# Kernel tuning notes

Hardware: AMD Instinct MI355X
Metric: run time of the kernel (lower is better)

## Reference

```python
import jax, jax.numpy as jnp
import numpy as np

N, E, H, NH, HD = 16384, 131072, 128, 8, 16
CUTOFF = 5.0
PATCH = H // 2  # 64, aggregation_custom effective patch dim


def setup_inputs() -> dict:
    key = jax.random.key(0)
    ks = jax.random.split(key, 24)
    w = lambda k, s: (jax.random.normal(k, s, dtype=jnp.float32) * 0.05)
    d = jax.random.normal(ks[5], (E, 3), dtype=jnp.float32)
    d = d / (jnp.linalg.norm(d, axis=-1, keepdims=True) + 1e-8)  # unit directions
    return {
        "x": jax.random.normal(ks[0], (N, H), dtype=jnp.float32),
        "vec": jax.random.normal(ks[1], (N, 3, H), dtype=jnp.float32),
        "edge_index": jax.random.randint(ks[2], (2, E), 0, N),
        "r_ij": jax.random.uniform(ks[3], (E,), dtype=jnp.float32) * CUTOFF,
        "f_ij": jax.random.normal(ks[4], (E, H), dtype=jnp.float32),
        "d_ij": d,
        "ln_g": jnp.ones((H,), jnp.float32), "ln_b": jnp.zeros((H,), jnp.float32),
        "Wq": w(ks[6], (H, H)), "bq": jnp.zeros((H,), jnp.float32),
        "Wk": w(ks[7], (H, H)), "bk": jnp.zeros((H,), jnp.float32),
        "Wv": w(ks[8], (H, H)), "bv": jnp.zeros((H,), jnp.float32),
        "Wdk": w(ks[9], (H, H)), "bdk": jnp.zeros((H,), jnp.float32),
        "Wdv": w(ks[10], (H, H)), "bdv": jnp.zeros((H,), jnp.float32),
        "Wvec": w(ks[11], (3 * H, H)),
        "Ws": w(ks[12], (2 * H, H)), "bs": jnp.zeros((2 * H,), jnp.float32),
        "Wo": w(ks[13], (3 * H, H)), "bo": jnp.zeros((3 * H,), jnp.float32),
        "Wf": w(ks[14], (H, H)), "bf": jnp.zeros((H,), jnp.float32),
        "Wwsrc": w(ks[15], (H, H)), "Wwtrg": w(ks[16], (H, H)),
        "Wagg": w(ks[17], (H, PATCH)),  # fc_all: Linear(64 -> 128, no bias)
        "agg_param": jnp.full((1,), 1e-5, dtype=jnp.float32),
    }


def _cutoff(r):
    return 0.5 * (jnp.cos(jnp.pi * r / CUTOFF) + 1.0) * (r < CUTOFF).astype(r.dtype)


def _vector_rejection(v, d):
    # v: [E,3,H], d: [E,3]
    proj = (v * d[:, :, None]).sum(axis=1, keepdims=True)  # [E,1,H]
    return v - proj * d[:, :, None]


def reference(x, vec, edge_index, r_ij, f_ij, d_ij, ln_g, ln_b,
              Wq, bq, Wk, bk, Wv, bv, Wdk, bdk, Wdv, bdv, Wvec,
              Ws, bs, Wo, bo, Wf, bf, Wwsrc, Wwtrg, Wagg, agg_param):
    silu = jax.nn.silu
    n = x.shape[0]
    # LayerNorm on x; VecLayerNorm with norm_type='none', trainable=False is identity
    mu = x.mean(-1, keepdims=True)
    var = ((x - mu) ** 2).mean(-1, keepdims=True)
    xn = (x - mu) / jnp.sqrt(var + 1e-5) * ln_g + ln_b

    q = (xn @ Wq.T + bq).reshape(n, NH, HD)
    k = (xn @ Wk.T + bk).reshape(n, NH, HD)
    v = (xn @ Wv.T + bv).reshape(n, NH, HD)
    dk = silu(f_ij @ Wdk.T + bdk).reshape(-1, NH, HD)
    dv = silu(f_ij @ Wdv.T + bdv).reshape(-1, NH, HD)

    vec1, vec2, vec3 = jnp.split(jnp.einsum('nch,oh->nco', vec, Wvec), 3, axis=-1)
    vec_dot = (vec1 * vec2).sum(axis=1)  # [N,H]

    src, dst = edge_index[0], edge_index[1]  # j, i
    # --- message ---
    attn = (q[dst] * k[src] * dk).sum(-1)                      # [E,NH]
    attn = silu(attn) * _cutoff(r_ij)[:, None]
    vmsg = (v[src] * dv * attn[:, :, None]).reshape(-1, H)     # [E,H]
    s1, s2 = jnp.split(silu(vmsg @ Ws.T + bs), 2, axis=1)
    vec_msg = vec[src] * s1[:, None, :] + s2[:, None, :] * d_ij[:, :, None]  # [E,3,H]

    # --- aggregation_custom on scalar messages ---
    e = vmsg.reshape(-1, 2, PATCH)                 # [E,2,64]
    ex = jnp.clip(jnp.einsum('epd,od->epo', e, Wagg), 0.0, 1.0)  # [E,2,128]
    gated = jnp.concatenate([(e * ex[:, :, :PATCH]).sum(1),
                             (e * ex[:, :, PATCH:]).sum(1)], axis=-1)  # [E,128]
    x_orig = jax.ops.segment_sum(vmsg, dst, num_segments=n)
    x_gate = jax.ops.segment_sum(gated, dst, num_segments=n)
    x_agg = jnp.abs(agg_param) * x_gate + x_orig
    vec_agg = jax.ops.segment_sum(vec_msg.reshape(-1, 3 * H), dst, num_segments=n).reshape(n, 3, H)

    # --- update ---
    o1, o2, o3 = jnp.split(x_agg @ Wo.T + bo, 3, axis=1)
    dx = vec_dot * o2 + o3
    dvec = vec3 * o1[:, None, :] + vec_agg

    # --- edge_update ---
    w1 = _vector_rejection(jnp.einsum('ech,oh->eco', vec[dst], Wwtrg), d_ij)
    w2 = _vector_rejection(jnp.einsum('ech,oh->eco', vec[src], Wwsrc), -d_ij)
    w_dot = (w1 * w2).sum(axis=1)  # [E,H]
    df_ij = silu(f_ij @ Wf.T + bf) * w_dot
    return dx, dvec, df_ij
```

## Files before the change

kernel.cpp:

```cpp
#include <hip/hip_runtime.h>

#define NN 16384
#define NE 131072
#define HH 128

typedef unsigned short u16;
typedef unsigned int u32;
typedef __attribute__((ext_vector_type(8))) short short8;
typedef __attribute__((ext_vector_type(4))) float f32x4;
typedef __attribute__((ext_vector_type(2))) float f32x2;
typedef __attribute__((ext_vector_type(2))) u32 u32x2;

__device__ __forceinline__ float b2f(u16 u){ u32 i=((u32)u)<<16; float f; __builtin_memcpy(&f,&i,4); return f; }
__device__ __forceinline__ u16 f2b(float f){ u32 i; __builtin_memcpy(&i,&f,4); u32 r=(i+0x7fffu+((i>>16)&1u))>>16; return (u16)r; }
__device__ __forceinline__ float blo(u32 v){ return b2f((u16)(v&0xffffu)); }
__device__ __forceinline__ float bhi(u32 v){ return b2f((u16)(v>>16)); }
__device__ __forceinline__ u32 pk(float a, float b){ return (u32)f2b(a) | ((u32)f2b(b)<<16); }
__device__ __forceinline__ float siluf(float x){ return x/(1.f+__expf(-x)); }

#define PBASE 58720256u
enum : unsigned {
  O_Wq=PBASE+0, O_Wk=PBASE+16384, O_Wv=PBASE+32768, O_Wdk=PBASE+49152,
  O_Wdv=PBASE+65536, O_Wf=PBASE+81920, O_Wwsrc=PBASE+98304, O_Wwtrg=PBASE+114688,
  O_Wvec=PBASE+131072, O_Ws=PBASE+180224, O_Wo=PBASE+212992, O_Wagg=PBASE+262144,
  O_bq=PBASE+270336, O_bk=PBASE+270464, O_bv=PBASE+270592, O_bdk=PBASE+270720,
  O_bdv=PBASE+270848, O_bs=PBASE+270976, O_bo=PBASE+271232, O_bf=PBASE+271616,
  O_lng=PBASE+271744, O_lnb=PBASE+271872, O_agg=PBASE+272000
};
#define CNT_OFF 117985280u
#define CUR_OFF 118050816u
#define SE_OFF  118116352u

struct Seg { const float* s; u32 off; u32 n; };
struct Pack { Seg d[25]; int cnt; };

__global__ __launch_bounds__(256) void k_cvt(Pack p, u16* __restrict__ base){
  int tid = blockIdx.x*blockDim.x + threadIdx.x;
  int stride = gridDim.x*blockDim.x;
  for (int s=0; s<p.cnt; ++s){
    const float* src = p.d[s].s;
    u16* dst = base + p.d[s].off;
    int n = (int)p.d[s].n, n4 = n>>2;
    const f32x4* s4 = (const f32x4*)src;
    for (int i=tid; i<n4; i+=stride){
      f32x4 v = s4[i];
      u32x2 o; o[0] = pk(v[0], v[1]); o[1] = pk(v[2], v[3]);
      *(u32x2*)(dst + 4*(size_t)i) = o;
    }
    for (int i = n4*4 + tid; i < n; i += stride) dst[i] = f2b(src[i]);
  }
}

__global__ __launch_bounds__(256) void k_hist(const int* __restrict__ ei, int* __restrict__ cnt){
  int e = blockIdx.x*256 + threadIdx.x;
  atomicAdd(&cnt[ei[NE + e]], 1);
}
__global__ __launch_bounds__(1024) void k_scan(const int* __restrict__ cnt, int* __restrict__ cur){
  __shared__ int part[1024];
  int t = threadIdx.x;
  int base = t*16;
  int local[16]; int s = 0;
#pragma unroll
  for (int k=0;k<16;++k){ local[k] = cnt[base+k]; s += local[k]; }
  part[t] = s;
  __syncthreads();
  for (int d=1; d<1024; d<<=1){
    int v = (t>=d) ? part[t-d] : 0;
    __syncthreads();
    part[t] += v;
    __syncthreads();
  }
  int run = (t>0) ? part[t-1] : 0;
#pragma unroll
  for (int k=0;k<16;++k){ cur[base+k] = run; run += local[k]; }
}
__global__ __launch_bounds__(256) void k_place(const int* __restrict__ ei, int* __restrict__ cur,
                                               int* __restrict__ se){
  int e = blockIdx.x*256 + threadIdx.x;
  int p = atomicAdd(&cur[ei[NE + e]], 1);
  se[p] = e;
}

template<int NK>
__device__ __forceinline__ f32x4 mm16(const u16* A, int lda, const u16* W, int ldw, f32x4 acc){
  int lane = threadIdx.x & 63;
  const u16* pa = A + (lane & 15)*lda + ((lane>>4)<<3);
  const u16* pw = W + (lane & 15)*ldw + ((lane>>4)<<3);
#pragma unroll
  for (int kc = 0; kc < NK; ++kc){
    short8 a = *(const short8*)(pa + kc*32);
    short8 b = *(const short8*)(pw + kc*32);
    acc = __builtin_amdgcn_mfma_f32_16x16x32_bf16(a, b, acc, 0, 0, 0);
  }
  return acc;
}

__global__ __launch_bounds__(256) void k_ln(const float* __restrict__ x, const u16* __restrict__ pb,
                                            u16* __restrict__ xn){
  int wid = threadIdx.x>>6, lane = threadIdx.x & 63;
  int n = blockIdx.x*4 + wid;
  f32x2 v = *(const f32x2*)(x + (size_t)n*HH + 2*lane);
  float a0 = v[0], a1 = v[1];
  float s = a0 + a1;
#pragma unroll
  for (int m=32; m; m>>=1) s += __shfl_xor(s, m);
  float mu = s*(1.f/128.f);
  float d0 = a0-mu, d1 = a1-mu;
  float vs = d0*d0 + d1*d1;
#pragma unroll
  for (int m=32; m; m>>=1) vs += __shfl_xor(vs, m);
  float rs = rsqrtf(vs*(1.f/128.f) + 1e-5f);
  u32 gg = *(const u32*)(pb + O_lng + 2*lane);
  u32 bb = *(const u32*)(pb + O_lnb + 2*lane);
  *(u32*)(xn + (size_t)n*HH + 2*lane) = pk(d0*rs*blo(gg)+blo(bb), d1*rs*bhi(gg)+bhi(bb));
}

__global__ __launch_bounds__(256) void k_gemm_qkv(const u16* __restrict__ xn,
    const u16* __restrict__ pb, u16* __restrict__ qkv){
  int wid = threadIdx.x>>6, lane = threadIdx.x & 63;
  int ct = blockIdx.y*4 + wid;
  int r0 = blockIdx.x*16;
  unsigned wo, bo_;
  if (ct < 8)      { wo = O_Wq; bo_ = O_bq; }
  else if (ct <16) { wo = O_Wk; bo_ = O_bk; }
  else             { wo = O_Wv; bo_ = O_bv; }
  int c0 = (ct & 7)*16;
  f32x4 acc = {0,0,0,0};
  acc = mm16<4>(xn + (size_t)r0*HH, HH, pb + wo + c0*HH, HH, acc);
  int col = ct*16 + (lane & 15);
  float bb = b2f(pb[bo_ + c0 + (lane&15)]);
#pragma unroll
  for (int j=0;j<4;++j){
    int r = r0 + ((lane>>4)<<2) + j;
    qkv[(size_t)r*384 + col] = f2b(acc[j] + bb);
  }
}

__global__ __launch_bounds__(256) void k_gemm_vec(const float* __restrict__ vecf,
    const u16* __restrict__ pb,
    u16* __restrict__ v12, u16* __restrict__ vec3, u16* __restrict__ Y){
  __shared__ u16 At[16*128];
  int tid = threadIdx.x, wid = tid>>6, lane = tid & 63;
  int r0 = blockIdx.x*16;
  {
    const float* src = vecf + (size_t)r0*HH;
    for (int i = tid*4; i < 2048; i += 1024){
      f32x4 v = *(const f32x4*)(src + i);
      u32x2 o; o[0] = pk(v[0], v[1]); o[1] = pk(v[2], v[3]);
      *(u32x2*)(At + i) = o;
    }
  }
  __syncthreads();
  for (int ct = wid; ct < 40; ct += 4){
    unsigned wo; int wc0;
    if (ct < 24)      { wo = O_Wvec;  wc0 = ct*16; }
    else if (ct < 32) { wo = O_Wwsrc; wc0 = (ct-24)*16; }
    else              { wo = O_Wwtrg; wc0 = (ct-32)*16; }
    f32x4 acc = {0,0,0,0};
    acc = mm16<4>(At, HH, pb + wo + wc0*HH, HH, acc);
    u16* dst; int ldc, dc0;
    if (ct < 16)      { dst = v12;  ldc = 256; dc0 = ct*16; }
    else if (ct < 24) { dst = vec3; ldc = 128; dc0 = (ct-16)*16; }
    else if (ct < 32) { dst = Y;    ldc = 256; dc0 = (ct-24)*16; }
    else              { dst = Y;    ldc = 256; dc0 = (ct-32)*16 + 128; }
    int col = dc0 + (lane & 15);
#pragma unroll
    for (int j=0;j<4;++j){
      int r = r0 + ((lane>>4)<<2) + j;
      dst[(size_t)r*ldc + col] = f2b(acc[j]);
    }
  }
}

__global__ __launch_bounds__(256) void k_edge(const float* __restrict__ f_ij,
    const u16* __restrict__ pb,
    const u16* __restrict__ qkv, const u16* __restrict__ Y,
    const int* __restrict__ ei, const int* __restrict__ se,
    const float* __restrict__ r_ij, const float* __restrict__ d_ij,
    const float* __restrict__ vecf, const float* __restrict__ aggf,
    float* __restrict__ df, float* __restrict__ xacc, float* __restrict__ vacc){
  __shared__ u16 fs[64*128];
  __shared__ u16 g2s[64*256];
  int tid = threadIdx.x, wid = tid>>6, lane = tid & 63;
  int t0 = blockIdx.x*64;
  int ereg=0, dreg=0, sreg=0;
  if (lane < 16){
    ereg = se[t0 + wid*16 + lane];
    dreg = ei[NE + ereg];
    sreg = ei[ereg];
  }
#pragma unroll
  for (int pass=0; pass<8; ++pass){
    int idx = pass*256 + lane*4;
    int rloc = idx >> 7, col = idx & 127;
    int er = __shfl(ereg, rloc);
    f32x4 v = *(const f32x4*)(f_ij + (size_t)er*HH + col);
    u32x2 o; o[0]=pk(v[0],v[1]); o[1]=pk(v[2],v[3]);
    *(u32x2*)(fs + (wid*16 + rloc)*HH + col) = o;
  }
  {
    const u16* pa = fs + (size_t)(wid*16 + (lane&15))*HH + ((lane>>4)<<3);
    short8 a0 = *(const short8*)(pa);
    short8 a1 = *(const short8*)(pa + 32);
    short8 a2 = *(const short8*)(pa + 64);
    short8 a3 = *(const short8*)(pa + 96);
    for (int ct=0; ct<16; ++ct){
      unsigned wo  = (ct<8) ? O_Wdk : O_Wdv;
      unsigned bo_ = (ct<8) ? O_bdk : O_bdv;
      int c0 = (ct&7)*16;
      const u16* pw = pb + wo + (size_t)(c0 + (lane&15))*HH + ((lane>>4)<<3);
      f32x4 acc = {0,0,0,0};
      acc = __builtin_amdgcn_mfma_f32_16x16x32_bf16(a0, *(const short8*)(pw),      acc, 0,0,0);
      acc = __builtin_amdgcn_mfma_f32_16x16x32_bf16(a1, *(const short8*)(pw + 32), acc, 0,0,0);
      acc = __builtin_amdgcn_mfma_f32_16x16x32_bf16(a2, *(const short8*)(pw + 64), acc, 0,0,0);
      acc = __builtin_amdgcn_mfma_f32_16x16x32_bf16(a3, *(const short8*)(pw + 96), acc, 0,0,0);
      float bb = b2f(pb[bo_ + c0 + (lane&15)]);
#pragma unroll
      for (int j=0;j<4;++j){
        int r = wid*16 + ((lane>>4)<<2) + j;
        g2s[r*256 + ct*16 + (lane&15)] = f2b(siluf(acc[j] + bb));
      }
    }
    f32x4 ffa[8];
#pragma unroll
    for (int cf=0; cf<8; ++cf){
      const u16* pw = pb + O_Wf + (size_t)(cf*16 + (lane&15))*HH + ((lane>>4)<<3);
      f32x4 acc = {0,0,0,0};
      acc = __builtin_amdgcn_mfma_f32_16x16x32_bf16(a0, *(const short8*)(pw),      acc, 0,0,0);
      acc = __builtin_amdgcn_mfma_f32_16x16x32_bf16(a1, *(const short8*)(pw + 32), acc, 0,0,0);
      acc = __builtin_amdgcn_mfma_f32_16x16x32_bf16(a2, *(const short8*)(pw + 64), acc, 0,0,0);
      acc = __builtin_amdgcn_mfma_f32_16x16x32_bf16(a3, *(const short8*)(pw + 96), acc, 0,0,0);
      ffa[cf] = acc;
    }
#pragma unroll
    for (int cf=0; cf<8; ++cf){
      float bb = b2f(pb[O_bf + cf*16 + (lane&15)]);
#pragma unroll
      for (int j=0;j<4;++j){
        int r = wid*16 + ((lane>>4)<<2) + j;
        fs[r*HH + cf*16 + (lane&15)] = f2b(siluf(ffa[cf][j] + bb));
      }
    }
  }
  int h0 = 2*lane;
  {
    int pdst = -1; u32 qq=0, ya0=0, ya1=0, ya2=0;
    for (int i=0;i<16;++i){
      int el = wid*16 + i;
      int e   = __shfl(ereg, i);
      int dst = __shfl(dreg, i);
      int src = __shfl(sreg, i);
      if (dst != pdst){
        qq  = *(const u32*)(qkv + (size_t)dst*384 + h0);
        ya0 = *(const u32*)(Y + ((size_t)dst*3+0)*256 + 128 + h0);
        ya1 = *(const u32*)(Y + ((size_t)dst*3+1)*256 + 128 + h0);
        ya2 = *(const u32*)(Y + ((size_t)dst*3+2)*256 + 128 + h0);
        pdst = dst;
      }
      u32 kk = *(const u32*)(qkv + (size_t)src*384 + 128 + h0);
      u32 vv = *(const u32*)(qkv + (size_t)src*384 + 256 + h0);
      u32 dk = *(const u32*)(g2s + el*256 + h0);
      u32 dv = *(const u32*)(g2s + el*256 + 128 + h0);
      u32 ff = *(const u32*)(fs  + el*HH + h0);
      float p = blo(qq)*blo(kk)*blo(dk) + bhi(qq)*bhi(kk)*bhi(dk);
      p += __shfl_xor(p,1); p += __shfl_xor(p,2); p += __shfl_xor(p,4);
      float r = r_ij[e];
      float cut = 0.5f*(__cosf(0.6283185307f*r)+1.f) * (r < 5.f ? 1.f : 0.f);
      float attn = siluf(p)*cut;
      float m0 = blo(vv)*blo(dv)*attn, m1 = bhi(vv)*bhi(dv)*attn;
      float ab0=0,ab1=0, ad0=0,ad1=0, bd0=0,bd1=0, ss=0;
      u32 ya[3] = {ya0, ya1, ya2};
#pragma unroll
      for (int c=0;c<3;++c){
        u32 bv2 = *(const u32*)(Y + ((size_t)src*3+c)*256 + h0);
        float dc = d_ij[(size_t)e*3+c];
        ab0 += blo(ya[c])*blo(bv2); ab1 += bhi(ya[c])*bhi(bv2);
        ad0 += blo(ya[c])*dc;       ad1 += bhi(ya[c])*dc;
        bd0 += blo(bv2)*dc;         bd1 += bhi(bv2)*dc;
        ss  += dc*dc;
      }
      float t = 2.f - ss;
      f32x2 dfo; dfo[0] = blo(ff)*(ab0 - ad0*bd0*t); dfo[1] = bhi(ff)*(ab1 - ad1*bd1*t);
      *(f32x2*)(df + (size_t)e*HH + h0) = dfo;
      *(u32*)(fs + el*HH + h0) = pk(m0, m1);
    }
  }
  float absA = fabsf(aggf[0]);
#pragma unroll
  for (int rr=0; rr<2; ++rr){
    int rt = wid*2 + rr;
    int el2 = wid*16 + 8*rr + ((lane&15)>>1);
    const u16* pa2 = fs + (size_t)el2*HH + ((lane&15)&1)*64 + ((lane>>4)<<3);
    short8 b0 = *(const short8*)(pa2);
    short8 b1 = *(const short8*)(pa2 + 32);
    for (int ct=0; ct<8; ++ct){
      const u16* pw = pb + O_Wagg + (size_t)(ct*16 + (lane&15))*64 + ((lane>>4)<<3);
      f32x4 acc = {0,0,0,0};
      acc = __builtin_amdgcn_mfma_f32_16x16x32_bf16(b0, *(const short8*)(pw),      acc, 0,0,0);
      acc = __builtin_amdgcn_mfma_f32_16x16x32_bf16(b1, *(const short8*)(pw + 32), acc, 0,0,0);
#pragma unroll
      for (int j=0;j<4;++j){
        int r = rt*16 + ((lane>>4)<<2) + j;
        g2s[r*128 + ct*16 + (lane&15)] = f2b(fminf(fmaxf(acc[j],0.f),1.f));
      }
    }
  }
  {
    int rdst = -1; float xc0=0.f, xc1=0.f;
    for (int i=0;i<16;++i){
      int el = wid*16 + i;
      int dst = __shfl(dreg, i);
      if (dst != rdst){
        if (rdst >= 0){
          atomicAdd(&xacc[(size_t)rdst*HH + h0],     xc0);
          atomicAdd(&xacc[(size_t)rdst*HH + h0 + 1], xc1);
        }
        rdst = dst; xc0 = xc1 = 0.f;
      }
      u32 mm = *(const u32*)(fs + el*HH + h0);
      u32 ml = *(const u32*)(fs + el*HH + (h0 & 63));
      u32 mh = *(const u32*)(fs + el*HH + 64 + (h0 & 63));
      u32 ex0 = *(const u32*)(g2s + (2*el)*128 + h0);
      u32 ex1 = *(const u32*)(g2s + (2*el+1)*128 + h0);
      xc0 += blo(mm) + absA*(blo(ml)*blo(ex0) + blo(mh)*blo(ex1));
      xc1 += bhi(mm) + absA*(bhi(ml)*bhi(ex0) + bhi(mh)*bhi(ex1));
    }
    if (rdst >= 0){
      atomicAdd(&xacc[(size_t)rdst*HH + h0],     xc0);
      atomicAdd(&xacc[(size_t)rdst*HH + h0 + 1], xc1);
    }
  }
  {
    const u16* ps = fs + (size_t)(wid*16 + (lane&15))*HH + ((lane>>4)<<3);
    short8 sa0 = *(const short8*)(ps);
    short8 sa1 = *(const short8*)(ps + 32);
    short8 sa2 = *(const short8*)(ps + 64);
    short8 sa3 = *(const short8*)(ps + 96);
    for (int ct=0; ct<16; ++ct){
      const u16* pw = pb + O_Ws + (size_t)(ct*16 + (lane&15))*HH + ((lane>>4)<<3);
      f32x4 acc = {0,0,0,0};
      acc = __builtin_amdgcn_mfma_f32_16x16x32_bf16(sa0, *(const short8*)(pw),      acc, 0,0,0);
      acc = __builtin_amdgcn_mfma_f32_16x16x32_bf16(sa1, *(const short8*)(pw + 32), acc, 0,0,0);
      acc = __builtin_amdgcn_mfma_f32_16x16x32_bf16(sa2, *(const short8*)(pw + 64), acc, 0,0,0);
      acc = __builtin_amdgcn_mfma_f32_16x16x32_bf16(sa3, *(const short8*)(pw + 96), acc, 0,0,0);
      float bb = b2f(pb[O_bs + ct*16 + (lane&15)]);
#pragma unroll
      for (int j=0;j<4;++j){
        int r = wid*16 + ((lane>>4)<<2) + j;
        g2s[r*256 + ct*16 + (lane&15)] = f2b(siluf(acc[j] + bb));
      }
    }
  }
  {
    int rdst = -1;
    float vc00=0.f,vc01=0.f, vc10=0.f,vc11=0.f, vc20=0.f,vc21=0.f;
    for (int i=0;i<16;++i){
      int el = wid*16 + i;
      int e   = __shfl(ereg, i);
      int dst = __shfl(dreg, i);
      int src = __shfl(sreg, i);
      if (dst != rdst){
        if (rdst >= 0){
          atomicAdd(&vacc[((size_t)rdst*3+0)*HH + h0],     vc00);
          atomicAdd(&vacc[((size_t)rdst*3+0)*HH + h0 + 1], vc01);
          atomicAdd(&vacc[((size_t)rdst*3+1)*HH + h0],     vc10);
          atomicAdd(&vacc[((size_t)rdst*3+1)*HH + h0 + 1], vc11);
          atomicAdd(&vacc[((size_t)rdst*3+2)*HH + h0],     vc20);
          atomicAdd(&vacc[((size_t)rdst*3+2)*HH + h0 + 1], vc21);
        }
        rdst = dst;
        vc00=vc01=vc10=vc11=vc20=vc21=0.f;
      }
      u32 s1 = *(const u32*)(g2s + el*256 + h0);
      u32 s2 = *(const u32*)(g2s + el*256 + 128 + h0);
      f32x2 vv0 = *(const f32x2*)(vecf + ((size_t)src*3+0)*HH + h0);
      f32x2 vv1 = *(const f32x2*)(vecf + ((size_t)src*3+1)*HH + h0);
      f32x2 vv2 = *(const f32x2*)(vecf + ((size_t)src*3+2)*HH + h0);
      float dc0 = d_ij[(size_t)e*3+0], dc1 = d_ij[(size_t)e*3+1], dc2 = d_ij[(size_t)e*3+2];
      vc00 += vv0[0]*blo(s1) + blo(s2)*dc0;  vc01 += vv0[1]*bhi(s1) + bhi(s2)*dc0;
      vc10 += vv1[0]*blo(s1) + blo(s2)*dc1;  vc11 += vv1[1]*bhi(s1) + bhi(s2)*dc1;
      vc20 += vv2[0]*blo(s1) + blo(s2)*dc2;  vc21 += vv2[1]*bhi(s1) + bhi(s2)*dc2;
    }
    if (rdst >= 0){
      atomicAdd(&vacc[((size_t)rdst*3+0)*HH + h0],     vc00);
      atomicAdd(&vacc[((size_t)rdst*3+0)*HH + h0 + 1], vc01);
      atomicAdd(&vacc[((size_t)rdst*3+1)*HH + h0],     vc10);
      atomicAdd(&vacc[((size_t)rdst*3+1)*HH + h0 + 1], vc11);
      atomicAdd(&vacc[((size_t)rdst*3+2)*HH + h0],     vc20);
      atomicAdd(&vacc[((size_t)rdst*3+2)*HH + h0 + 1], vc21);
    }
  }
}

__global__ __launch_bounds__(256) void k_update(const float* __restrict__ xacc,
    const u16* __restrict__ pb, const u16* __restrict__ v12, const u16* __restrict__ vec3,
    const float* __restrict__ vacc,
    float* __restrict__ dx, float* __restrict__ dvec){
  int wid = threadIdx.x>>6, lane = threadIdx.x & 63;
  int ct = blockIdx.y*4 + wid;
  int r0 = blockIdx.x*16;
  int c0 = ct*16;
  f32x4 a1 = {0,0,0,0}, a2 = {0,0,0,0}, a3 = {0,0,0,0};
  const float* pa = xacc + (size_t)(r0 + (lane&15))*HH + ((lane>>4)<<3);
#pragma unroll
  for (int kc=0; kc<4; ++kc){
    f32x4 f0 = *(const f32x4*)(pa + kc*32);
    f32x4 f1 = *(const f32x4*)(pa + kc*32 + 4);
    short8 av;
    av[0]=(short)f2b(f0[0]); av[1]=(short)f2b(f0[1]); av[2]=(short)f2b(f0[2]); av[3]=(short)f2b(f0[3]);
    av[4]=(short)f2b(f1[0]); av[5]=(short)f2b(f1[1]); av[6]=(short)f2b(f1[2]); av[7]=(short)f2b(f1[3]);
    const u16* pw = pb + O_Wo + (size_t)(c0 + (lane&15))*HH + ((lane>>4)<<3) + kc*32;
    short8 b1 = *(const short8*)(pw);
    short8 b2 = *(const short8*)(pw + 128*HH);
    short8 b3 = *(const short8*)(pw + 256*HH);
    a1 = __builtin_amdgcn_mfma_f32_16x16x32_bf16(av, b1, a1, 0,0,0);
    a2 = __builtin_amdgcn_mfma_f32_16x16x32_bf16(av, b2, a2, 0,0,0);
    a3 = __builtin_amdgcn_mfma_f32_16x16x32_bf16(av, b3, a3, 0,0,0);
  }
  int h = c0 + (lane & 15);
  float bo1 = b2f(pb[O_bo + h]), bo2 = b2f(pb[O_bo + 128 + h]), bo3 = b2f(pb[O_bo + 256 + h]);
#pragma unroll
  for (int j=0;j<4;++j){
    int r = r0 + ((lane>>4)<<2) + j;
    float o1 = a1[j]+bo1, o2 = a2[j]+bo2, o3 = a3[j]+bo3;
    float vdot = 0.f;
#pragma unroll
    for (int c=0;c<3;++c){
      const u16* row = v12 + ((size_t)r*3 + c)*256;
      vdot += b2f(row[h]) * b2f(row[128 + h]);
    }
    dx[(size_t)r*HH + h] = vdot*o2 + o3;
#pragma unroll
    for (int c=0;c<3;++c){
      size_t idx = ((size_t)r*3+c)*HH + h;
      dvec[idx] = b2f(vec3[idx])*o1 + vacc[idx];
    }
  }
}

extern "C" void kernel_launch(void* const* d_in, const int* in_sizes, int n_in,
                              void* d_out, int out_size, void* d_ws, size_t ws_size,
                              hipStream_t stream){
  (void)in_sizes; (void)n_in; (void)out_size; (void)ws_size;
  const float* x     = (const float*)d_in[0];
  const float* vecf  = (const float*)d_in[1];
  const int*   ei    = (const int*)d_in[2];
  const float* r_ij  = (const float*)d_in[3];
  const float* f_ij  = (const float*)d_in[4];
  const float* d_ij  = (const float*)d_in[5];
  const float* aggf  = (const float*)d_in[28];

  char* ws = (char*)d_ws;
  u16*   wsu   = (u16*)d_ws;
  float* xacc  = (float*)(ws + 0);
  float* vacc  = (float*)(ws + 8388608);
  u16*   Ybuf  = (u16*)(ws + 33554432);
  u16*   xn    = (u16*)(ws + 58720256);
  u16*   vec3  = (u16*)(ws + 67108864);
  u16*   qkv   = (u16*)(ws + 79691776);
  u16*   v12   = (u16*)(ws + 92274688);
  int*   cnt   = (int*)(ws + CNT_OFF);
  int*   cur   = (int*)(ws + CUR_OFF);
  int*   se    = (int*)(ws + SE_OFF);

  float* out  = (float*)d_out;
  float* dx   = out;
  float* dvec = out + (size_t)NN*128;
  float* df   = out + (size_t)NN*512;

  Pack p; int c = 0;
  auto add = [&](int idx, unsigned off, unsigned n){ p.d[c].s=(const float*)d_in[idx]; p.d[c].off=off; p.d[c].n=n; ++c; };
  add(8,  O_Wq,   16384); add(10, O_Wk,   16384); add(12, O_Wv,   16384);
  add(14, O_Wdk,  16384); add(16, O_Wdv,  16384); add(23, O_Wf,   16384);
  add(25, O_Wwsrc,16384); add(26, O_Wwtrg,16384);
  add(18, O_Wvec, 49152); add(19, O_Ws,   32768); add(21, O_Wo,   49152);
  add(27, O_Wagg,  8192);
  add(9,  O_bq, 128); add(11, O_bk, 128); add(13, O_bv, 128); add(15, O_bdk, 128);
  add(17, O_bdv, 128); add(20, O_bs, 256); add(22, O_bo, 384); add(24, O_bf, 128);
  add(6,  O_lng, 128); add(7,  O_lnb, 128); add(28, O_agg, 1);
  p.cnt = c;

  hipMemsetAsync(ws, 0, 33554432, stream);
  hipMemsetAsync(ws + CNT_OFF, 0, 65536, stream);
  k_hist<<<dim3(NE/256), 256, 0, stream>>>(ei, cnt);
  k_scan<<<dim3(1), 1024, 0, stream>>>(cnt, cur);
  k_place<<<dim3(NE/256), 256, 0, stream>>>(ei, cur, se);
  k_cvt<<<dim3(128), 256, 0, stream>>>(p, wsu);
  k_ln<<<dim3(NN/4), 256, 0, stream>>>(x, wsu, xn);
  k_gemm_qkv<<<dim3(NN/16, 6), 256, 0, stream>>>(xn, wsu, qkv);
  k_gemm_vec<<<dim3(3*NN/16), 256, 0, stream>>>(vecf, wsu, v12, vec3, Ybuf);
  k_edge<<<dim3(NE/64), 256, 0, stream>>>(f_ij, wsu, qkv, Ybuf, ei, se, r_ij, d_ij,
                                          vecf, aggf, df, xacc, vacc);
  k_update<<<dim3(NN/16, 2), 256, 0, stream>>>(xacc, wsu, v12, vec3, vacc, dx, dvec);
}
```

Before: 428.6 us.

## Shrink edge-kernel LDS to two swizzled buffers by staging GEMM outputs in phases

Cuts the edge kernel's shared memory from 48KB to 32KB by splitting the Wdk/Wdv, Wagg and Ws GEMMs into half-width phases that reuse one 64x128 buffer. Each phase is followed by its own consumption and atomic-scatter pass. It also applies an XOR swizzle to LDS addresses to reduce bank conflicts, adds may_alias types, compiler fences and full unrolling of the per-edge loops. In exchange there are extra scatter passes with more atomics, d_ij/vecf are reread, and register pressure rises from the hoisted A fragments and the per-edge attention arrays.

```diff
diff --git a/kernel.cpp b/kernel.cpp
--- a/kernel.cpp
+++ b/kernel.cpp
@@ -10,6 +10,12 @@
 typedef __attribute__((ext_vector_type(4))) float f32x4;
 typedef __attribute__((ext_vector_type(2))) float f32x2;
 typedef __attribute__((ext_vector_type(2))) u32 u32x2;
+typedef u16 __attribute__((may_alias)) u16a;
+typedef u32 __attribute__((may_alias)) u32a;
+typedef short8 __attribute__((may_alias)) short8a;
+typedef u32x2 __attribute__((may_alias)) u32x2a;
+
+#define CFENCE() asm volatile("" ::: "memory")
 
 __device__ __forceinline__ float b2f(u16 u){ u32 i=((u32)u)<<16; float f; __builtin_memcpy(&f,&i,4); return f; }
 __device__ __forceinline__ u16 f2b(float f){ u32 i; __builtin_memcpy(&i,&f,4); u32 r=(i+0x7fffu+((i>>16)&1u))>>16; return (u16)r; }
@@ -17,6 +23,12 @@
 __device__ __forceinline__ float bhi(u32 v){ return b2f((u16)(v>>16)); }
 __device__ __forceinline__ u32 pk(float a, float b){ return (u32)f2b(a) | ((u32)f2b(b)<<16); }
 __device__ __forceinline__ float siluf(float x){ return x/(1.f+__expf(-x)); }
+
+#define SW8(b) ((b) ^ ((((b)>>8)&7)<<4))
+__device__ __forceinline__ u32 ldsr32(const char* base, int b){ return *(const u32a*)(base + SW8(b)); }
+__device__ __forceinline__ void ldsw16(char* base, int b, u16 v){ *(u16a*)(base + SW8(b)) = v; }
+__device__ __forceinline__ short8 ldsr128(const char* base, int b){ return *(const short8a*)(base + SW8(b)); }
+__device__ __forceinline__ void ldsw64(char* base, int b, u32x2 v){ *(u32x2a*)(base + SW8(b)) = v; }
 
 #define PBASE 58720256u
 enum : unsigned {
@@ -45,7 +57,7 @@
     for (int i=tid; i<n4; i+=stride){
       f32x4 v = s4[i];
       u32x2 o; o[0] = pk(v[0], v[1]); o[1] = pk(v[2], v[3]);
-      *(u32x2*)(dst + 4*(size_t)i) = o;
+      *(u32x2a*)(dst + 4*(size_t)i) = o;
     }
     for (int i = n4*4 + tid; i < n; i += stride) dst[i] = f2b(src[i]);
   }
@@ -88,8 +100,8 @@
   const u16* pw = W + (lane & 15)*ldw + ((lane>>4)<<3);
 #pragma unroll
   for (int kc = 0; kc < NK; ++kc){
-    short8 a = *(const short8*)(pa + kc*32);
-    short8 b = *(const short8*)(pw + kc*32);
+    short8 a = *(const short8a*)(pa + kc*32);
+    short8 b = *(const short8a*)(pw + kc*32);
     acc = __builtin_amdgcn_mfma_f32_16x16x32_bf16(a, b, acc, 0, 0, 0);
   }
   return acc;
@@ -110,9 +122,9 @@
 #pragma unroll
   for (int m=32; m; m>>=1) vs += __shfl_xor(vs, m);
   float rs = rsqrtf(vs*(1.f/128.f) + 1e-5f);
-  u32 gg = *(const u32*)(pb + O_lng + 2*lane);
-  u32 bb = *(const u32*)(pb + O_lnb + 2*lane);
-  *(u32*)(xn + (size_t)n*HH + 2*lane) = pk(d0*rs*blo(gg)+blo(bb), d1*rs*bhi(gg)+bhi(bb));
+  u32 gg = *(const u32a*)(pb + O_lng + 2*lane);
+  u32 bb = *(const u32a*)(pb + O_lnb + 2*lane);
+  *(u32a*)(xn + (size_t)n*HH + 2*lane) = pk(d0*rs*blo(gg)+blo(bb), d1*rs*bhi(gg)+bhi(bb));
 }
 
 __global__ __launch_bounds__(256) void k_gemm_qkv(const u16* __restrict__ xn,
@@ -147,7 +159,7 @@
     for (int i = tid*4; i < 2048; i += 1024){
       f32x4 v = *(const f32x4*)(src + i);
       u32x2 o; o[0] = pk(v[0], v[1]); o[1] = pk(v[2], v[3]);
-      *(u32x2*)(At + i) = o;
+      *(u32x2a*)(At + i) = o;
     }
   }
   __syncthreads();
@@ -179,8 +191,10 @@
     const float* __restrict__ r_ij, const float* __restrict__ d_ij,
     const float* __restrict__ vecf, const float* __restrict__ aggf,
     float* __restrict__ df, float* __restrict__ xacc, float* __restrict__ vacc){
-  __shared__ u16 fs[64*128];
-  __shared__ u16 g2s[64*256];
+  __shared__ u16 fsA[64*128];
+  __shared__ u16 fsB[64*128];
+  char* fsb = (char*)fsA;
+  char* bsb = (char*)fsB;
   int tid = threadIdx.x, wid = tid>>6, lane = tid & 63;
   int t0 = blockIdx.x*64;
   int ereg=0, dreg=0, sreg=0;
@@ -189,6 +203,7 @@
     dreg = ei[NE + ereg];
     sreg = ei[ereg];
   }
+  int h0 = 2*lane;
 #pragma unroll
   for (int pass=0; pass<8; ++pass){
     int idx = pass*256 + lane*4;
@@ -196,117 +211,146 @@
     int er = __shfl(ereg, rloc);
     f32x4 v = *(const f32x4*)(f_ij + (size_t)er*HH + col);
     u32x2 o; o[0]=pk(v[0],v[1]); o[1]=pk(v[2],v[3]);
-    *(u32x2*)(fs + (wid*16 + rloc)*HH + col) = o;
-  }
-  {
-    const u16* pa = fs + (size_t)(wid*16 + (lane&15))*HH + ((lane>>4)<<3);
-    short8 a0 = *(const short8*)(pa);
-    short8 a1 = *(const short8*)(pa + 32);
-    short8 a2 = *(const short8*)(pa + 64);
-    short8 a3 = *(const short8*)(pa + 96);
-    for (int ct=0; ct<16; ++ct){
-      unsigned wo  = (ct<8) ? O_Wdk : O_Wdv;
-      unsigned bo_ = (ct<8) ? O_bdk : O_bdv;
-      int c0 = (ct&7)*16;
-      const u16* pw = pb + wo + (size_t)(c0 + (lane&15))*HH + ((lane>>4)<<3);
-      f32x4 acc = {0,0,0,0};
-      acc = __builtin_amdgcn_mfma_f32_16x16x32_bf16(a0, *(const short8*)(pw),      acc, 0,0,0);
-      acc = __builtin_amdgcn_mfma_f32_16x16x32_bf16(a1, *(const short8*)(pw + 32), acc, 0,0,0);
-      acc = __builtin_amdgcn_mfma_f32_16x16x32_bf16(a2, *(const short8*)(pw + 64), acc, 0,0,0);
-      acc = __builtin_amdgcn_mfma_f32_16x16x32_bf16(a3, *(const short8*)(pw + 96), acc, 0,0,0);
-      float bb = b2f(pb[bo_ + c0 + (lane&15)]);
-#pragma unroll
-      for (int j=0;j<4;++j){
-        int r = wid*16 + ((lane>>4)<<2) + j;
-        g2s[r*256 + ct*16 + (lane&15)] = f2b(siluf(acc[j] + bb));
-      }
-    }
-    f32x4 ffa[8];
-#pragma unroll
-    for (int cf=0; cf<8; ++cf){
-      const u16* pw = pb + O_Wf + (size_t)(cf*16 + (lane&15))*HH + ((lane>>4)<<3);
-      f32x4 acc = {0,0,0,0};
-      acc = __builtin_amdgcn_mfma_f32_16x16x32_bf16(a0, *(const short8*)(pw),      acc, 0,0,0);
-      acc = __builtin_amdgcn_mfma_f32_16x16x32_bf16(a1, *(const short8*)(pw + 32), acc, 0,0,0);
-      acc = __builtin_amdgcn_mfma_f32_16x16x32_bf16(a2, *(const short8*)(pw + 64), acc, 0,0,0);
-      acc = __builtin_amdgcn_mfma_f32_16x16x32_bf16(a3, *(const short8*)(pw + 96), acc, 0,0,0);
-      ffa[cf] = acc;
-    }
-#pragma unroll
-    for (int cf=0; cf<8; ++cf){
-      float bb = b2f(pb[O_bf + cf*16 + (lane&15)]);
-#pragma unroll
-      for (int j=0;j<4;++j){
-        int r = wid*16 + ((lane>>4)<<2) + j;
-        fs[r*HH + cf*16 + (lane&15)] = f2b(siluf(ffa[cf][j] + bb));
-      }
-    }
-  }
-  int h0 = 2*lane;
+    ldsw64(fsb, (wid*16 + rloc)*256 + col*2, o);
+  }
+  CFENCE();
+  int ab = (wid*16 + (lane&15))*256 + ((lane>>4)<<4);
+  short8 a0 = ldsr128(fsb, ab);
+  short8 a1 = ldsr128(fsb, ab + 64);
+  short8 a2 = ldsr128(fsb, ab + 128);
+  short8 a3 = ldsr128(fsb, ab + 192);
+  CFENCE();
+#pragma unroll
+  for (int cf=0; cf<8; ++cf){
+    const u16* pw = pb + O_Wf + (size_t)(cf*16 + (lane&15))*HH + ((lane>>4)<<3);
+    f32x4 acc = {0,0,0,0};
+    acc = __builtin_amdgcn_mfma_f32_16x16x32_bf16(a0, *(const short8a*)(pw),      acc, 0,0,0);
+    acc = __builtin_amdgcn_mfma_f32_16x16x32_bf16(a1, *(const short8a*)(pw + 32), acc, 0,0,0);
+    acc = __builtin_amdgcn_mfma_f32_16x16x32_bf16(a2, *(const short8a*)(pw + 64), acc, 0,0,0);
+    acc = __builtin_amdgcn_mfma_f32_16x16x32_bf16(a3, *(const short8a*)(pw + 96), acc, 0,0,0);
+    float bb = b2f(pb[O_bf + cf*16 + (lane&15)]);
+#pragma unroll
+    for (int j=0;j<4;++j){
+      int r = wid*16 + ((lane>>4)<<2) + j;
+      ldsw16(fsb, r*256 + (cf*16 + (lane&15))*2, f2b(siluf(acc[j] + bb)));
+    }
+  }
+  CFENCE();
+#pragma unroll
+  for (int ct=0; ct<8; ++ct){
+    const u16* pw = pb + O_Wdk + (size_t)(ct*16 + (lane&15))*HH + ((lane>>4)<<3);
+    f32x4 acc = {0,0,0,0};
+    acc = __builtin_amdgcn_mfma_f32_16x16x32_bf16(a0, *(const short8a*)(pw),      acc, 0,0,0);
+    acc = __builtin_amdgcn_mfma_f32_16x16x32_bf16(a1, *(const short8a*)(pw + 32), acc, 0,0,0);
+    acc = __builtin_amdgcn_mfma_f32_16x16x32_bf16(a2, *(const short8a*)(pw + 64), acc, 0,0,0);
+    acc = __builtin_amdgcn_mfma_f32_16x16x32_bf16(a3, *(const short8a*)(pw + 96), acc, 0,0,0);
+    float bb = b2f(pb[O_bdk + ct*16 + (lane&15)]);
+#pragma unroll
+    for (int j=0;j<4;++j){
+      int r = wid*16 + ((lane>>4)<<2) + j;
+      ldsw16(bsb, r*256 + (ct*16 + (lane&15))*2, f2b(siluf(acc[j] + bb)));
+    }
+  }
+  CFENCE();
+  float attn_r[16];
+  u32 vvr[16];
   {
     int pdst = -1; u32 qq=0, ya0=0, ya1=0, ya2=0;
+#pragma unroll
     for (int i=0;i<16;++i){
       int el = wid*16 + i;
       int e   = __shfl(ereg, i);
       int dst = __shfl(dreg, i);
       int src = __shfl(sreg, i);
       if (dst != pdst){
-        qq  = *(const u32*)(qkv + (size_t)dst*384 + h0);
-        ya0 = *(const u32*)(Y + ((size_t)dst*3+0)*256 + 128 + h0);
-        ya1 = *(const u32*)(Y + ((size_t)dst*3+1)*256 + 128 + h0);
-        ya2 = *(const u32*)(Y + ((size_t)dst*3+2)*256 + 128 + h0);
+        qq  = *(const u32a*)(qkv + (size_t)dst*384 + h0);
+        ya0 = *(const u32a*)(Y + ((size_t)dst*3+0)*256 + 128 + h0);
+        ya1 = *(const u32a*)(Y + ((size_t)dst*3+1)*256 + 128 + h0);
+        ya2 = *(const u32a*)(Y + ((size_t)dst*3+2)*256 + 128 + h0);
         pdst = dst;
       }
-      u32 kk = *(const u32*)(qkv + (size_t)src*384 + 128 + h0);
-      u32 vv = *(const u32*)(qkv + (size_t)src*384 + 256 + h0);
-      u32 dk = *(const u32*)(g2s + el*256 + h0);
-      u32 dv = *(const u32*)(g2s + el*256 + 128 + h0);
-      u32 ff = *(const u32*)(fs  + el*HH + h0);
+      u32 kk  = *(const u32a*)(qkv + (size_t)src*384 + 128 + h0);
+      u32 vv  = *(const u32a*)(qkv + (size_t)src*384 + 256 + h0);
+      u32 yb0 = *(const u32a*)(Y + ((size_t)src*3+0)*256 + h0);
+      u32 yb1 = *(const u32a*)(Y + ((size_t)src*3+1)*256 + h0);
+      u32 yb2 = *(const u32a*)(Y + ((size_t)src*3+2)*256 + h0);
+      float r   = r_ij[e];
+      float dc0 = d_ij[(size_t)e*3+0];
+      float dc1 = d_ij[(size_t)e*3+1];
+      float dc2 = d_ij[(size_t)e*3+2];
+      u32 dk = ldsr32(bsb, el*256 + h0*2);
+      u32 ff = ldsr32(fsb, el*256 + h0*2);
       float p = blo(qq)*blo(kk)*blo(dk) + bhi(qq)*bhi(kk)*bhi(dk);
       p += __shfl_xor(p,1); p += __shfl_xor(p,2); p += __shfl_xor(p,4);
-      float r = r_ij[e];
       float cut = 0.5f*(__cosf(0.6283185307f*r)+1.f) * (r < 5.f ? 1.f : 0.f);
-      float attn = siluf(p)*cut;
-      float m0 = blo(vv)*blo(dv)*attn, m1 = bhi(vv)*bhi(dv)*attn;
-      float ab0=0,ab1=0, ad0=0,ad1=0, bd0=0,bd1=0, ss=0;
-      u32 ya[3] = {ya0, ya1, ya2};
-#pragma unroll
-      for (int c=0;c<3;++c){
-        u32 bv2 = *(const u32*)(Y + ((size_t)src*3+c)*256 + h0);
-        float dc = d_ij[(size_t)e*3+c];
-        ab0 += blo(ya[c])*blo(bv2); ab1 += bhi(ya[c])*bhi(bv2);
-        ad0 += blo(ya[c])*dc;       ad1 += bhi(ya[c])*dc;
-        bd0 += blo(bv2)*dc;         bd1 += bhi(bv2)*dc;
-        ss  += dc*dc;
-      }
+      attn_r[i] = siluf(p)*cut;
+      vvr[i] = vv;
+      float ab0,ab1, ad0,ad1, bd0,bd1, ss;
+      ab0 = blo(ya0)*blo(yb0); ab1 = bhi(ya0)*bhi(yb0);
+      ad0 = blo(ya0)*dc0;      ad1 = bhi(ya0)*dc0;
+      bd0 = blo(yb0)*dc0;      bd1 = bhi(yb0)*dc0;
+      ss  = dc0*dc0;
+      ab0 += blo(ya1)*blo(yb1); ab1 += bhi(ya1)*bhi(yb1);
+      ad0 += blo(ya1)*dc1;      ad1 += bhi(ya1)*dc1;
+      bd0 += blo(yb1)*dc1;      bd1 += bhi(yb1)*dc1;
+      ss  += dc1*dc1;
+      ab0 += blo(ya2)*blo(yb2); ab1 += bhi(ya2)*bhi(yb2);
+      ad0 += blo(ya2)*dc2;      ad1 += bhi(ya2)*dc2;
+      bd0 += blo(yb2)*dc2;      bd1 += bhi(yb2)*dc2;
+      ss  += dc2*dc2;
       float t = 2.f - ss;
       f32x2 dfo; dfo[0] = blo(ff)*(ab0 - ad0*bd0*t); dfo[1] = bhi(ff)*(ab1 - ad1*bd1*t);
       *(f32x2*)(df + (size_t)e*HH + h0) = dfo;
-      *(u32*)(fs + el*HH + h0) = pk(m0, m1);
-    }
-  }
+    }
+  }
+  CFENCE();
+#pragma unroll
+  for (int ct=0; ct<8; ++ct){
+    const u16* pw = pb + O_Wdv + (size_t)(ct*16 + (lane&15))*HH + ((lane>>4)<<3);
+    f32x4 acc = {0,0,0,0};
+    acc = __builtin_amdgcn_mfma_f32_16x16x32_bf16(a0, *(const short8a*)(pw),      acc, 0,0,0);
+    acc = __builtin_amdgcn_mfma_f32_16x16x32_bf16(a1, *(const short8a*)(pw + 32), acc, 0,0,0);
+    acc = __builtin_amdgcn_mfma_f32_16x16x32_bf16(a2, *(const short8a*)(pw + 64), acc, 0,0,0);
+    acc = __builtin_amdgcn_mfma_f32_16x16x32_bf16(a3, *(const short8a*)(pw + 96), acc, 0,0,0);
+    float bb = b2f(pb[O_bdv + ct*16 + (lane&15)]);
+#pragma unroll
+    for (int j=0;j<4;++j){
+      int r = wid*16 + ((lane>>4)<<2) + j;
+      ldsw16(bsb, r*256 + (ct*16 + (lane&15))*2, f2b(siluf(acc[j] + bb)));
+    }
+  }
+  CFENCE();
+#pragma unroll
+  for (int i=0;i<16;++i){
+    int el = wid*16 + i;
+    u32 dv = ldsr32(bsb, el*256 + h0*2);
+    float m0 = blo(vvr[i])*blo(dv)*attn_r[i];
+    float m1 = bhi(vvr[i])*bhi(dv)*attn_r[i];
+    *(u32a*)(fsb + SW8(el*256 + h0*2)) = pk(m0, m1);
+  }
+  CFENCE();
   float absA = fabsf(aggf[0]);
-#pragma unroll
-  for (int rr=0; rr<2; ++rr){
-    int rt = wid*2 + rr;
-    int el2 = wid*16 + 8*rr + ((lane&15)>>1);
-    const u16* pa2 = fs + (size_t)el2*HH + ((lane&15)&1)*64 + ((lane>>4)<<3);
-    short8 b0 = *(const short8*)(pa2);
-    short8 b1 = *(const short8*)(pa2 + 32);
-    for (int ct=0; ct<8; ++ct){
-      const u16* pw = pb + O_Wagg + (size_t)(ct*16 + (lane&15))*64 + ((lane>>4)<<3);
-      f32x4 acc = {0,0,0,0};
-      acc = __builtin_amdgcn_mfma_f32_16x16x32_bf16(b0, *(const short8*)(pw),      acc, 0,0,0);
-      acc = __builtin_amdgcn_mfma_f32_16x16x32_bf16(b1, *(const short8*)(pw + 32), acc, 0,0,0);
-#pragma unroll
-      for (int j=0;j<4;++j){
-        int r = rt*16 + ((lane>>4)<<2) + j;
-        g2s[r*128 + ct*16 + (lane&15)] = f2b(fminf(fmaxf(acc[j],0.f),1.f));
-      }
-    }
-  }
+  short8 sa0 = ldsr128(fsb, ab);
+  short8 sa1 = ldsr128(fsb, ab + 64);
+  short8 sa2 = ldsr128(fsb, ab + 128);
+  short8 sa3 = ldsr128(fsb, ab + 192);
+  CFENCE();
+#pragma unroll
+  for (int ct=0; ct<8; ++ct){
+    const u16* pw = pb + O_Wagg + (size_t)(ct*16 + (lane&15))*64 + ((lane>>4)<<3);
+    f32x4 acc = {0,0,0,0};
+    acc = __builtin_amdgcn_mfma_f32_16x16x32_bf16(sa0, *(const short8a*)(pw),      acc, 0,0,0);
+    acc = __builtin_amdgcn_mfma_f32_16x16x32_bf16(sa1, *(const short8a*)(pw + 32), acc, 0,0,0);
+#pragma unroll
+    for (int j=0;j<4;++j){
+      int r = wid*16 + ((lane>>4)<<2) + j;
+      ldsw16(bsb, r*256 + (ct*16 + (lane&15))*2, f2b(fminf(fmaxf(acc[j],0.f),1.f)));
+    }
+  }
+  CFENCE();
   {
     int rdst = -1; float xc0=0.f, xc1=0.f;
+#pragma unroll
     for (int i=0;i<16;++i){
       int el = wid*16 + i;
       int dst = __shfl(dreg, i);
@@ -317,46 +361,77 @@
         }
         rdst = dst; xc0 = xc1 = 0.f;
       }
-      u32 mm = *(const u32*)(fs + el*HH + h0);
-      u32 ml = *(const u32*)(fs + el*HH + (h0 & 63));
-      u32 mh = *(const u32*)(fs + el*HH + 64 + (h0 & 63));
-      u32 ex0 = *(const u32*)(g2s + (2*el)*128 + h0);
-      u32 ex1 = *(const u32*)(g2s + (2*el+1)*128 + h0);
-      xc0 += blo(mm) + absA*(blo(ml)*blo(ex0) + blo(mh)*blo(ex1));
-      xc1 += bhi(mm) + absA*(bhi(ml)*bhi(ex0) + bhi(mh)*bhi(ex1));
+      u32 mm  = ldsr32(fsb, el*256 + h0*2);
+      u32 ml  = ldsr32(fsb, el*256 + (h0&63)*2);
+      u32 ex0 = ldsr32(bsb, el*256 + h0*2);
+      xc0 += blo(mm) + absA*blo(ml)*blo(ex0);
+      xc1 += bhi(mm) + absA*bhi(ml)*bhi(ex0);
     }
     if (rdst >= 0){
       atomicAdd(&xacc[(size_t)rdst*HH + h0],     xc0);
       atomicAdd(&xacc[(size_t)rdst*HH + h0 + 1], xc1);
     }
   }
+  CFENCE();
+#pragma unroll
+  for (int ct=0; ct<8; ++ct){
+    const u16* pw = pb + O_Wagg + (size_t)(ct*16 + (lane&15))*64 + ((lane>>4)<<3);
+    f32x4 acc = {0,0,0,0};
+    acc = __builtin_amdgcn_mfma_f32_16x16x32_bf16(sa2, *(const short8a*)(pw),      acc, 0,0,0);
+    acc = __builtin_amdgcn_mfma_f32_16x16x32_bf16(sa3, *(const short8a*)(pw + 32), acc, 0,0,0);
+#pragma unroll
+    for (int j=0;j<4;++j){
+      int r = wid*16 + ((lane>>4)<<2) + j;
+      ldsw16(bsb, r*256 + (ct*16 + (lane&15))*2, f2b(fminf(fmaxf(acc[j],0.f),1.f)));
+    }
+  }
+  CFENCE();
   {
-    const u16* ps = fs + (size_t)(wid*16 + (lane&15))*HH + ((lane>>4)<<3);
-    short8 sa0 = *(const short8*)(ps);
-    short8 sa1 = *(const short8*)(ps + 32);
-    short8 sa2 = *(const short8*)(ps + 64);
-    short8 sa3 = *(const short8*)(ps + 96);
-    for (int ct=0; ct<16; ++ct){
-      const u16* pw = pb + O_Ws + (size_t)(ct*16 + (lane&15))*HH + ((lane>>4)<<3);
-      f32x4 acc = {0,0,0,0};
-      acc = __builtin_amdgcn_mfma_f32_16x16x32_bf16(sa0, *(const short8*)(pw),      acc, 0,0,0);
-      acc = __builtin_amdgcn_mfma_f32_16x16x32_bf16(sa1, *(const short8*)(pw + 32), acc, 0,0,0);
-      acc = __builtin_amdgcn_mfma_f32_16x16x32_bf16(sa2, *(const short8*)(pw + 64), acc, 0,0,0);
-      acc = __builtin_amdgcn_mfma_f32_16x16x32_bf16(sa3, *(const short8*)(pw + 96), acc, 0,0,0);
-      float bb = b2f(pb[O_bs + ct*16 + (lane&15)]);
-#pragma unroll
-      for (int j=0;j<4;++j){
-        int r = wid*16 + ((lane>>4)<<2) + j;
-        g2s[r*256 + ct*16 + (lane&15)] = f2b(siluf(acc[j] + bb));
+    int rdst = -1; float xc0=0.f, xc1=0.f;
+#pragma unroll
+    for (int i=0;i<16;++i){
+      int el = wid*16 + i;
+      int dst = __shfl(dreg, i);
+      if (dst != rdst){
+        if (rdst >= 0){
+          atomicAdd(&xacc[(size_t)rdst*HH + h0],     xc0);
+          atomicAdd(&xacc[(size_t)rdst*HH + h0 + 1], xc1);
+        }
+        rdst = dst; xc0 = xc1 = 0.f;
       }
-    }
-  }
+      u32 mh  = ldsr32(fsb, el*256 + 128 + (h0&63)*2);
+      u32 ex1 = ldsr32(bsb, el*256 + h0*2);
+      xc0 += absA*blo(mh)*blo(ex1);
+      xc1 += absA*bhi(mh)*bhi(ex1);
+    }
+    if (rdst >= 0){
+      atomicAdd(&xacc[(size_t)rdst*HH + h0],     xc0);
+      atomicAdd(&xacc[(size_t)rdst*HH + h0 + 1], xc1);
+    }
+  }
+  CFENCE();
+#pragma unroll
+  for (int ct=0; ct<8; ++ct){
+    const u16* pw = pb + O_Ws + (size_t)(ct*16 + (lane&15))*HH + ((lane>>4)<<3);
+    f32x4 acc = {0,0,0,0};
+    acc = __builtin_amdgcn_mfma_f32_16x16x32_bf16(sa0, *(const short8a*)(pw),      acc, 0,0,0);
+    acc = __builtin_amdgcn_mfma_f32_16x16x32_bf16(sa1, *(const short8a*)(pw + 32), acc, 0,0,0);
+    acc = __builtin_amdgcn_mfma_f32_16x16x32_bf16(sa2, *(const short8a*)(pw + 64), acc, 0,0,0);
+    acc = __builtin_amdgcn_mfma_f32_16x16x32_bf16(sa3, *(const short8a*)(pw + 96), acc, 0,0,0);
+    float bb = b2f(pb[O_bs + ct*16 + (lane&15)]);
+#pragma unroll
+    for (int j=0;j<4;++j){
+      int r = wid*16 + ((lane>>4)<<2) + j;
+      ldsw16(bsb, r*256 + (ct*16 + (lane&15))*2, f2b(siluf(acc[j] + bb)));
+    }
+  }
+  CFENCE();
   {
     int rdst = -1;
     float vc00=0.f,vc01=0.f, vc10=0.f,vc11=0.f, vc20=0.f,vc21=0.f;
+#pragma unroll
     for (int i=0;i<16;++i){
       int el = wid*16 + i;
-      int e   = __shfl(ereg, i);
       int dst = __shfl(dreg, i);
       int src = __shfl(sreg, i);
       if (dst != rdst){
@@ -371,15 +446,67 @@
         rdst = dst;
         vc00=vc01=vc10=vc11=vc20=vc21=0.f;
       }
-      u32 s1 = *(const u32*)(g2s + el*256 + h0);
-      u32 s2 = *(const u32*)(g2s + el*256 + 128 + h0);
+      u32 s1 = ldsr32(bsb, el*256 + h0*2);
       f32x2 vv0 = *(const f32x2*)(vecf + ((size_t)src*3+0)*HH + h0);
       f32x2 vv1 = *(const f32x2*)(vecf + ((size_t)src*3+1)*HH + h0);
       f32x2 vv2 = *(const f32x2*)(vecf + ((size_t)src*3+2)*HH + h0);
-      float dc0 = d_ij[(size_t)e*3+0], dc1 = d_ij[(size_t)e*3+1], dc2 = d_ij[(size_t)e*3+2];
-      vc00 += vv0[0]*blo(s1) + blo(s2)*dc0;  vc01 += vv0[1]*bhi(s1) + bhi(s2)*dc0;
-      vc10 += vv1[0]*blo(s1) + blo(s2)*dc1;  vc11 += vv1[1]*bhi(s1) + bhi(s2)*dc1;
-      vc20 += vv2[0]*blo(s1) + blo(s2)*dc2;  vc21 += vv2[1]*bhi(s1) + bhi(s2)*dc2;
+      vc00 += vv0[0]*blo(s1);  vc01 += vv0[1]*bhi(s1);
+      vc10 += vv1[0]*blo(s1);  vc11 += vv1[1]*bhi(s1);
+      vc20 += vv2[0]*blo(s1);  vc21 += vv2[1]*bhi(s1);
+    }
+    if (rdst >= 0){
+      atomicAdd(&vacc[((size_t)rdst*3+0)*HH + h0],     vc00);
+      atomicAdd(&vacc[((size_t)rdst*3+0)*HH + h0 + 1], vc01);
+      atomicAdd(&vacc[((size_t)rdst*3+1)*HH + h0],     vc10);
+      atomicAdd(&vacc[((size_t)rdst*3+1)*HH + h0 + 1], vc11);
+      atomicAdd(&vacc[((size_t)rdst*3+2)*HH + h0],     vc20);
+      atomicAdd(&vacc[((size_t)rdst*3+2)*HH + h0 + 1], vc21);
+    }
+  }
+  CFENCE();
+#pragma unroll
+  for (int ct=0; ct<8; ++ct){
+    const u16* pw = pb + O_Ws + (size_t)(128 + ct*16 + (lane&15))*HH + ((lane>>4)<<3);
+    f32x4 acc = {0,0,0,0};
+    acc = __builtin_amdgcn_mfma_f32_16x16x32_bf16(sa0, *(const short8a*)(pw),      acc, 0,0,0);
+    acc = __builtin_amdgcn_mfma_f32_16x16x32_bf16(sa1, *(const short8a*)(pw + 32), acc, 0,0,0);
+    acc = __builtin_amdgcn_mfma_f32_16x16x32_bf16(sa2, *(const short8a*)(pw + 64), acc, 0,0,0);
+    acc = __builtin_amdgcn_mfma_f32_16x16x32_bf16(sa3, *(const short8a*)(pw + 96), acc, 0,0,0);
+    float bb = b2f(pb[O_bs + 128 + ct*16 + (lane&15)]);
+#pragma unroll
+    for (int j=0;j<4;++j){
+      int r = wid*16 + ((lane>>4)<<2) + j;
+      ldsw16(bsb, r*256 + (ct*16 + (lane&15))*2, f2b(siluf(acc[j] + bb)));
+    }
+  }
+  CFENCE();
+  {
+    int rdst = -1;
+    float vc00=0.f,vc01=0.f, vc10=0.f,vc11=0.f, vc20=0.f,vc21=0.f;
+#pragma unroll
+    for (int i=0;i<16;++i){
+      int el = wid*16 + i;
+      int e   = __shfl(ereg, i);
+      int dst = __shfl(dreg, i);
+      if (dst != rdst){
+        if (rdst >= 0){
+          atomicAdd(&vacc[((size_t)rdst*3+0)*HH + h0],     vc00);
+          atomicAdd(&vacc[((size_t)rdst*3+0)*HH + h0 + 1], vc01);
+          atomicAdd(&vacc[((size_t)rdst*3+1)*HH + h0],     vc10);
+          atomicAdd(&vacc[((size_t)rdst*3+1)*HH + h0 + 1], vc11);
+          atomicAdd(&vacc[((size_t)rdst*3+2)*HH + h0],     vc20);
+          atomicAdd(&vacc[((size_t)rdst*3+2)*HH + h0 + 1], vc21);
+        }
+        rdst = dst;
+        vc00=vc01=vc10=vc11=vc20=vc21=0.f;
+      }
+      u32 s2 = ldsr32(bsb, el*256 + h0*2);
+      float dc0 = d_ij[(size_t)e*3+0];
+      float dc1 = d_ij[(size_t)e*3+1];
+      float dc2 = d_ij[(size_t)e*3+2];
+      vc00 += blo(s2)*dc0;  vc01 += bhi(s2)*dc0;
+      vc10 += blo(s2)*dc1;  vc11 += bhi(s2)*dc1;
+      vc20 += blo(s2)*dc2;  vc21 += bhi(s2)*dc2;
     }
     if (rdst >= 0){
       atomicAdd(&vacc[((size_t)rdst*3+0)*HH + h0],     vc00);
@@ -410,9 +537,9 @@
     av[0]=(short)f2b(f0[0]); av[1]=(short)f2b(f0[1]); av[2]=(short)f2b(f0[2]); av[3]=(short)f2b(f0[3]);
     av[4]=(short)f2b(f1[0]); av[5]=(short)f2b(f1[1]); av[6]=(short)f2b(f1[2]); av[7]=(short)f2b(f1[3]);
     const u16* pw = pb + O_Wo + (size_t)(c0 + (lane&15))*HH + ((lane>>4)<<3) + kc*32;
-    short8 b1 = *(const short8*)(pw);
-    short8 b2 = *(const short8*)(pw + 128*HH);
-    short8 b3 = *(const short8*)(pw + 256*HH);
+    short8 b1 = *(const short8a*)(pw);
+    short8 b2 = *(const short8a*)(pw + 128*HH);
+    short8 b3 = *(const short8a*)(pw + 256*HH);
     a1 = __builtin_amdgcn_mfma_f32_16x16x32_bf16(av, b1, a1, 0,0,0);
     a2 = __builtin_amdgcn_mfma_f32_16x16x32_bf16(av, b2, a2, 0,0,0);
     a3 = __builtin_amdgcn_mfma_f32_16x16x32_bf16(av, b3, a3, 0,0,0);
```

Result: slower. 465.6 us (+8.6%).
